# Kernel optimization log

Measured on AMD Instinct MI355X. Metric: run time of the kernel, lower is better.

The kernel has to match this reference:

```python
import jax, jax.numpy as jnp
import numpy as np

B, S, E = 2, 2048, 2048
H, KV, D = 16, 4, 128
G = H // KV
ROPE_THETA = 10000.0


def setup_inputs() -> dict:
    key = jax.random.key(0)
    ks = jax.random.split(key, 8)
    std = 0.02
    return {
        "x": jax.random.normal(ks[0], (B, S, E), jnp.float32),
        "Wq": jax.random.normal(ks[1], (H * D, E), jnp.float32) * std,
        "bq": jax.random.normal(ks[2], (H * D,), jnp.float32) * std,
        "Wk": jax.random.normal(ks[3], (KV * D, E), jnp.float32) * std,
        "bk": jax.random.normal(ks[4], (KV * D,), jnp.float32) * std,
        "Wv": jax.random.normal(ks[5], (KV * D, E), jnp.float32) * std,
        "bv": jax.random.normal(ks[6], (KV * D,), jnp.float32) * std,
        "Wo": jax.random.normal(ks[7], (E, H * D), jnp.float32) * std,
    }


def _rope_cos_sin(seq_len, head_dim):
    inv_freq = 1.0 / (ROPE_THETA ** (jnp.arange(0, head_dim, 2, dtype=jnp.float32) / head_dim))
    pos = jnp.arange(seq_len, dtype=jnp.float32)  # rope scale factor = 1.0
    freqs = pos[:, None] * inv_freq[None, :]        # [S, D/2]
    emb = jnp.concatenate([freqs, freqs], axis=-1)  # [S, D]
    return jnp.cos(emb), jnp.sin(emb)


def _apply_rope(t, cos, sin):
    # t: [..., S, <extra dims>, D]; cos/sin: [S, D] broadcast over extra dims
    half = t.shape[-1] // 2
    extra = t.ndim - 3  # dims between S (axis 1) and D (last)
    c = cos.reshape((1, cos.shape[0]) + (1,) * extra + (cos.shape[1],))
    s = sin.reshape((1, sin.shape[0]) + (1,) * extra + (sin.shape[1],))
    rot = jnp.concatenate([-t[..., half:], t[..., :half]], axis=-1)
    return t * c + rot * s


def reference(x, Wq, bq, Wk, bk, Wv, bv, Wo):
    b, s, e = x.shape
    # QKV projections (biases on q/k/v, none on o)
    q = (jnp.einsum("bse,he->bsh", x, Wq) + bq).reshape(b, s, KV, G, D)
    k = (jnp.einsum("bse,he->bsh", x, Wk) + bk).reshape(b, s, KV, D)
    v = (jnp.einsum("bse,he->bsh", x, Wv) + bv).reshape(b, s, KV, D)

    cos, sin = _rope_cos_sin(s, D)
    q = _apply_rope(q, cos, sin)
    k = _apply_rope(k, cos, sin)

    scale = 1.0 / jnp.sqrt(jnp.float32(D))
    # GQA: q heads grouped per kv head; k/v broadcast over group dim
    scores = jnp.einsum("bskgd,btkd->bkgst", q, k) * scale  # [B,KV,G,S,S]
    causal = jnp.tril(jnp.ones((s, s), dtype=bool))
    scores = jnp.where(causal, scores, jnp.float32(-1e9))
    attn = jax.nn.softmax(scores, axis=-1)
    out = jnp.einsum("bkgst,btkd->bskgd", attn, v).reshape(b, s, H * D)
    return jnp.einsum("bsh,eh->bse", out, Wo)
```

## Files before the change

### kernel.cpp

```cpp
#include <hip/hip_runtime.h>
#include <hip/hip_bf16.h>
#include <math.h>

#define BB 2
#define SS 2048
#define EE 2048
#define HH 16
#define KVH 4
#define DD 128
#define QTILES 32

typedef short short8 __attribute__((ext_vector_type(8)));
typedef float f32x4 __attribute__((ext_vector_type(4)));

__device__ __forceinline__ unsigned int f2bf1(float x) {
    union { float f; unsigned int u; } v; v.f = x;
    return (v.u + 0x7FFFu + ((v.u >> 16) & 1u)) >> 16;
}
__device__ __forceinline__ unsigned int packbf(float a, float b) {
    return f2bf1(a) | (f2bf1(b) << 16);
}
__device__ __forceinline__ void gl_lds16(const void* g, void* l) {
    __builtin_amdgcn_global_load_lds(
        (const __attribute__((address_space(1))) unsigned int*)g,
        (__attribute__((address_space(3))) unsigned int*)l,
        16, 0, 0);
}

__global__ __launch_bounds__(256) void cvt_all_kernel(
    const float* __restrict__ x,  const float* __restrict__ Wq,
    const float* __restrict__ Wk, const float* __restrict__ Wv,
    const float* __restrict__ Wo, const float* __restrict__ bq,
    const float* __restrict__ bk, const float* __restrict__ bv,
    unsigned short* __restrict__ xb, unsigned short* __restrict__ wqkv,
    unsigned short* __restrict__ wob, float* __restrict__ bqkv,
    float* __restrict__ rtab)
{
    long id = (long)blockIdx.x * 256 + threadIdx.x;
    const float* src; unsigned short* dst; long j;
    if (id < 2097152)      { j = id;           src = x;  dst = xb; }
    else if (id < 3145728) { j = id - 2097152; src = Wq; dst = wqkv; }
    else if (id < 3407872) { j = id - 3145728; src = Wk; dst = wqkv + 4194304; }
    else if (id < 3670016) { j = id - 3407872; src = Wv; dst = wqkv + 5242880; }
    else if (id < 4718592) { j = id - 3670016; src = Wo; dst = wob; }
    else if (id < 4719360) {
        long c = (id - 4718592) * 4;
#pragma unroll
        for (int e = 0; e < 4; ++e) {
            long cc = c + e;
            bqkv[cc] = (cc < 2048) ? bq[cc] : (cc < 2560 ? bk[cc - 2048] : bv[cc - 2560]);
        }
        return;
    } else if (id < 4850432) {
        long e = id - 4719360;
        int sg = (int)(e >> 6);
        int dg = (int)(e & 63);
        float inv_freq = expf(-(float)dg * (logf(10000.0f) / 64.0f));
        float fr = (float)sg * inv_freq;
        rtab[e]          = cosf(fr);
        rtab[131072 + e] = sinf(fr);
        return;
    } else return;
    float4 f = ((const float4*)src)[j];
    ((uint2*)dst)[j] = make_uint2(packbf(f.x, f.y), packbf(f.z, f.w));
}

template <bool OUT_BF16>
__global__ __launch_bounds__(256) void gemm_mfma_kernel(
    const unsigned short* __restrict__ A, const unsigned short* __restrict__ W,
    const float* __restrict__ bias, void* __restrict__ Cout,
    int M, int N, int K)
{
    __shared__ unsigned short As[128 * 32];
    __shared__ unsigned short Bs[128 * 32];

    const int tid  = threadIdx.x;
    const int w    = tid >> 6;
    const int lane = tid & 63;
    const int quad = lane >> 4;
    const int l16  = lane & 15;
    const int wr   = w >> 1, wc = w & 1;
    const int m0 = blockIdx.y * 128, n0 = blockIdx.x * 128;

    f32x4 acc[4][4];
#pragma unroll
    for (int i = 0; i < 4; ++i)
#pragma unroll
        for (int j = 0; j < 4; ++j) acc[i][j] = (f32x4){0.f, 0.f, 0.f, 0.f};

    const unsigned short* Ag = A + (size_t)(m0 + w * 32 + (lane >> 2)) * K + (lane & 3) * 8;
    const unsigned short* Wg = W + (size_t)(n0 + w * 32 + (lane >> 2)) * K + (lane & 3) * 8;
    unsigned short* AsB = &As[(w * 32) * 32];
    unsigned short* BsB = &Bs[(w * 32) * 32];

    for (int k0 = 0; k0 < K; k0 += 32) {
        gl_lds16(Ag + k0, AsB);
        gl_lds16(Ag + k0 + (size_t)16 * K, AsB + 16 * 32);
        gl_lds16(Wg + k0, BsB);
        gl_lds16(Wg + k0 + (size_t)16 * K, BsB + 16 * 32);
        __syncthreads();

        short8 a_f[4], b_f[4];
#pragma unroll
        for (int i = 0; i < 4; ++i)
            a_f[i] = *(const short8*)&As[(wr * 64 + i * 16 + l16) * 32 + quad * 8];
#pragma unroll
        for (int j = 0; j < 4; ++j)
            b_f[j] = *(const short8*)&Bs[(wc * 64 + j * 16 + l16) * 32 + quad * 8];
#pragma unroll
        for (int i = 0; i < 4; ++i)
#pragma unroll
            for (int j = 0; j < 4; ++j)
                acc[i][j] = __builtin_amdgcn_mfma_f32_16x16x32_bf16(a_f[i], b_f[j], acc[i][j], 0, 0, 0);
        __syncthreads();
    }

    float bj[4];
#pragma unroll
    for (int j = 0; j < 4; ++j)
        bj[j] = bias ? bias[n0 + wc * 64 + j * 16 + l16] : 0.0f;
#pragma unroll
    for (int i = 0; i < 4; ++i) {
#pragma unroll
        for (int r = 0; r < 4; ++r) {
            size_t row = m0 + wr * 64 + i * 16 + quad * 4 + r;
#pragma unroll
            for (int j = 0; j < 4; ++j) {
                size_t col = n0 + wc * 64 + j * 16 + l16;
                float val = acc[i][j][r] + bj[j];
                if (OUT_BF16)
                    ((unsigned short*)Cout)[row * N + col] = (unsigned short)f2bf1(val);
                else
                    ((float*)Cout)[row * N + col] = val;
            }
        }
    }
}

__global__ __launch_bounds__(256) void rope_kernel(
    unsigned short* __restrict__ qkv,
    const float* __restrict__ ctab, const float* __restrict__ stab)
{
    const int m = blockIdx.x;
    const int s = m & (SS - 1);
    unsigned short* p = qkv + (size_t)m * 3072;
    const float* cr = ctab + s * 64;
    const float* sr = stab + s * 64;
#pragma unroll
    for (int it = 0; it < 5; ++it) {
        int idx = threadIdx.x + it * 256;
        int hh = idx >> 6;
        int d  = idx & 63;
        int cb = (hh < 16) ? hh * 128 : 2048 + (hh - 16) * 128;
        float c  = cr[d];
        float sn = sr[d];
        union { unsigned int u; float f; } x1, x2;
        x1.u = ((unsigned int)p[cb + d]) << 16;
        x2.u = ((unsigned int)p[cb + d + 64]) << 16;
        p[cb + d]      = (unsigned short)f2bf1(x1.f * c - x2.f * sn);
        p[cb + d + 64] = (unsigned short)f2bf1(x2.f * c + x1.f * sn);
    }
}

__global__ __launch_bounds__(256, 2) void attn_mfma_kernel(
    const unsigned short* __restrict__ qkv, unsigned short* __restrict__ o)
{
    __shared__ unsigned int Ks_u[2][64 * 64];
    __shared__ unsigned int Vs_u[2][128 * 32];
    __shared__ unsigned short Ps[4][16 * 64];

    const int tid  = threadIdx.x;
    const int w    = tid >> 6;
    const int lane = tid & 63;
    const int quad = lane >> 4;
    const int l16  = lane & 15;
    const int jpair = blockIdx.x;
    const int h     = blockIdx.y;
    const int b     = blockIdx.z;
    const int kv    = h >> 2;

    const float k2 = 0.12752789744920764f;

    const unsigned short* kbase = qkv + (size_t)b * SS * 3072 + 2048 + kv * 128;
    const unsigned short* vbase = kbase + 512;

    const int kc  = tid & 15;
    const int kp0 = tid >> 4;
    const int vpp = tid >> 3;
    const int vd0 = (tid & 7) * 16;

    for (int pass = 0; pass < 2; ++pass) {
        const int qt = pass ? (QTILES - 1 - jpair) : jpair;
        const int q0 = qt * 64;

        short8 qf[4];
        {
            const unsigned short* qp = qkv + (size_t)(b * SS + q0 + w * 16 + l16) * 3072 + h * 128 + quad * 8;
#pragma unroll
            for (int ks = 0; ks < 4; ++ks)
                qf[ks] = *(const short8*)(qp + ks * 32);
        }

        uint4 kpre[4], vpa[2], vpb[2];
        {
            const unsigned short* kg = kbase + (size_t)kp0 * 3072 + kc * 8;
#pragma unroll
            for (int rr = 0; rr < 4; ++rr)
                kpre[rr] = *(const uint4*)(kg + (size_t)rr * 16 * 3072);
            const unsigned short* vg = vbase + (size_t)(2 * vpp) * 3072 + vd0;
            vpa[0] = *(const uint4*)(vg);
            vpa[1] = *(const uint4*)(vg + 8);
            vpb[0] = *(const uint4*)(vg + 3072);
            vpb[1] = *(const uint4*)(vg + 3072 + 8);
        }

        float m_r[4], l_r[4];
        f32x4 Oacc[8];
#pragma unroll
        for (int r = 0; r < 4; ++r) { m_r[r] = -1e30f; l_r[r] = 0.0f; }
#pragma unroll
        for (int ot = 0; ot < 8; ++ot) Oacc[ot] = (f32x4){0.f, 0.f, 0.f, 0.f};

        for (int t = 0; t <= qt; ++t) {
            const int buf = t & 1;
            unsigned int* Kb = Ks_u[buf];
            unsigned int* Vb = Vs_u[buf];

#pragma unroll
            for (int rr = 0; rr < 4; ++rr) {
                int pos = kp0 + rr * 16;
                int key = (kp0 + rr) & 7;
                *(uint4*)&Kb[pos * 64 + (kc ^ key) * 4] = kpre[rr];
            }
            {
                const unsigned int* pa = (const unsigned int*)vpa;
                const unsigned int* pb = (const unsigned int*)vpb;
#pragma unroll
                for (int j = 0; j < 8; ++j) {
                    unsigned lo = __builtin_amdgcn_perm(pb[j], pa[j], 0x05040100);
                    unsigned hi = __builtin_amdgcn_perm(pb[j], pa[j], 0x07060302);
                    int d0 = vd0 + 2 * j;
                    int g  = d0 >> 4;
                    int k0 = (d0 + g) & 7;
                    int k1 = (d0 + 1 + g) & 7;
                    Vb[d0 * 32 + (((vpp >> 2) ^ k0) & 7) * 4 + (vpp & 3)] = lo;
                    Vb[(d0 + 1) * 32 + (((vpp >> 2) ^ k1) & 7) * 4 + (vpp & 3)] = hi;
                }
            }

            if (t < qt) {
                const unsigned short* kg = kbase + (size_t)((t + 1) * 64 + kp0) * 3072 + kc * 8;
#pragma unroll
                for (int rr = 0; rr < 4; ++rr)
                    kpre[rr] = *(const uint4*)(kg + (size_t)rr * 16 * 3072);
                const unsigned short* vg = vbase + (size_t)((t + 1) * 64 + 2 * vpp) * 3072 + vd0;
                vpa[0] = *(const uint4*)(vg);
                vpa[1] = *(const uint4*)(vg + 8);
                vpb[0] = *(const uint4*)(vg + 3072);
                vpb[1] = *(const uint4*)(vg + 3072 + 8);
            }
            __syncthreads();

            f32x4 S[4];
#pragma unroll
            for (int ct = 0; ct < 4; ++ct) {
                f32x4 s = (f32x4){0.f, 0.f, 0.f, 0.f};
                const int row = ct * 16 + l16;
                const int key = (l16 + ct) & 7;
#pragma unroll
                for (int ks = 0; ks < 4; ++ks) {
                    short8 kf = *(const short8*)&Kb[row * 64 + ((ks * 4 + quad) ^ key) * 4];
                    s = __builtin_amdgcn_mfma_f32_16x16x32_bf16(qf[ks], kf, s, 0, 0, 0);
                }
                S[ct] = s;
            }

            if (t == qt) {
                const int rowloc = w * 16 + quad * 4;
#pragma unroll
                for (int ct = 0; ct < 4; ++ct)
#pragma unroll
                    for (int r = 0; r < 4; ++r)
                        if (ct * 16 + l16 > rowloc + r) S[ct][r] = -1e30f;
            }

#pragma unroll
            for (int r = 0; r < 4; ++r) {
                float c0 = fmaxf(fmaxf(S[0][r], S[1][r]), fmaxf(S[2][r], S[3][r]));
                c0 = fmaxf(c0, __shfl_xor(c0, 1));
                c0 = fmaxf(c0, __shfl_xor(c0, 2));
                c0 = fmaxf(c0, __shfl_xor(c0, 4));
                c0 = fmaxf(c0, __shfl_xor(c0, 8));
                float mnew = fmaxf(m_r[r], c0);
                float alpha = exp2f((m_r[r] - mnew) * k2);
                m_r[r] = mnew;
                float mh = mnew * k2;
                float rs = 0.0f;
                const int prow = quad * 4 + r;
                const int pkey = (prow >> 2) ^ ((prow & 3) << 1);
#pragma unroll
                for (int ct = 0; ct < 4; ++ct) {
                    float p = exp2f(S[ct][r] * k2 - mh);
                    rs += p;
                    int chunk = ct * 2 + (l16 >> 3);
                    union { float f; unsigned u; } pu; pu.f = p;
                    Ps[w][prow * 64 + (chunk ^ pkey) * 8 + (l16 & 7)] =
                        (unsigned short)((pu.u + 0x8000u) >> 16);
                }
                rs += __shfl_xor(rs, 1);
                rs += __shfl_xor(rs, 2);
                rs += __shfl_xor(rs, 4);
                rs += __shfl_xor(rs, 8);
                l_r[r] = l_r[r] * alpha + rs;
#pragma unroll
                for (int ot = 0; ot < 8; ++ot) Oacc[ot][r] *= alpha;
            }

            {
                const int pkeyr = (l16 >> 2) ^ ((l16 & 3) << 1);
                short8 pf0 = *(const short8*)&Ps[w][l16 * 64 + (quad ^ pkeyr) * 8];
                short8 pf1 = *(const short8*)&Ps[w][l16 * 64 + ((4 + quad) ^ pkeyr) * 8];
#pragma unroll
                for (int ot = 0; ot < 8; ++ot) {
                    const int d = ot * 16 + l16;
                    const int vkey = (l16 + ot) & 7;
                    short8 v0 = *(const short8*)&Vb[d * 32 + (quad ^ vkey) * 4];
                    Oacc[ot] = __builtin_amdgcn_mfma_f32_16x16x32_bf16(pf0, v0, Oacc[ot], 0, 0, 0);
                    short8 v1 = *(const short8*)&Vb[d * 32 + ((4 + quad) ^ vkey) * 4];
                    Oacc[ot] = __builtin_amdgcn_mfma_f32_16x16x32_bf16(pf1, v1, Oacc[ot], 0, 0, 0);
                }
            }
        }

        float inv[4];
#pragma unroll
        for (int r = 0; r < 4; ++r) inv[r] = 1.0f / l_r[r];
        const int orow0 = q0 + w * 16 + quad * 4;
        unsigned short* ob = o + (size_t)(b * SS + orow0) * 2048 + h * 128 + l16;
#pragma unroll
        for (int r = 0; r < 4; ++r)
#pragma unroll
            for (int ot = 0; ot < 8; ++ot)
                ob[(size_t)r * 2048 + ot * 16] = (unsigned short)f2bf1(Oacc[ot][r] * inv[r]);

        __syncthreads();
    }
}

extern "C" void kernel_launch(void* const* d_in, const int* in_sizes, int n_in,
                              void* d_out, int out_size, void* d_ws, size_t ws_size,
                              hipStream_t stream)
{
    const float* x  = (const float*)d_in[0];
    const float* Wq = (const float*)d_in[1];
    const float* bq = (const float*)d_in[2];
    const float* Wk = (const float*)d_in[3];
    const float* bk = (const float*)d_in[4];
    const float* Wv = (const float*)d_in[5];
    const float* bv = (const float*)d_in[6];
    const float* Wo = (const float*)d_in[7];
    float* out = (float*)d_out;

    const int M = BB * SS;
    char* wsb = (char*)d_ws;
    unsigned short* xb   = (unsigned short*)wsb;  wsb += (size_t)M * EE * 2;
    unsigned short* wqkv = (unsigned short*)wsb;  wsb += (size_t)3072 * EE * 2;
    unsigned short* wob  = (unsigned short*)wsb;  wsb += (size_t)EE * EE * 2;
    unsigned short* qkvb = (unsigned short*)wsb;  wsb += (size_t)M * 3072 * 2;
    unsigned short* abb  = (unsigned short*)wsb;  wsb += (size_t)M * 2048 * 2;
    float* bqkv = (float*)wsb;                    wsb += 4096 * 4;
    float* rtab = (float*)wsb;

    cvt_all_kernel<<<18947, 256, 0, stream>>>(x, Wq, Wk, Wv, Wo, bq, bk, bv,
                                              xb, wqkv, wob, bqkv, rtab);

    gemm_mfma_kernel<true><<<dim3(3072 / 128, M / 128), 256, 0, stream>>>(
        xb, wqkv, bqkv, qkvb, M, 3072, EE);

    rope_kernel<<<M, 256, 0, stream>>>(qkvb, rtab, rtab + 131072);

    attn_mfma_kernel<<<dim3(16, HH, BB), 256, 0, stream>>>(qkvb, abb);

    gemm_mfma_kernel<false><<<dim3(EE / 128, M / 128), 256, 0, stream>>>(
        abb, wob, nullptr, out, M, EE, 2048);
}
```

Measured before the change: 361.7 us.

## Split long causal query tiles across two blocks and merge partials

The paired-pass attention grid (16 blocks, each doing a short and a long query tile) becomes 48 blocks. The first 16 query tiles are handled whole, and the last 16 are split into two KV-range halves whose unnormalized outputs and max/sum stats are written to fp32 workspace. A new merge kernel combines each pair with log-sum-exp rescaling. The K/V LDS double buffer is also dropped to a single buffer with an extra barrier, which shrinks LDS use. The cost is an extra launch, fp32 partial traffic, and less overlap between loads and compute.

```diff
diff --git a/kernel.cpp b/kernel.cpp
--- a/kernel.cpp
+++ b/kernel.cpp
@@ -163,10 +163,11 @@
 }
 
 __global__ __launch_bounds__(256, 2) void attn_mfma_kernel(
-    const unsigned short* __restrict__ qkv, unsigned short* __restrict__ o)
-{
-    __shared__ unsigned int Ks_u[2][64 * 64];
-    __shared__ unsigned int Vs_u[2][128 * 32];
+    const unsigned short* __restrict__ qkv, unsigned short* __restrict__ o,
+    float* __restrict__ Opart, float* __restrict__ mlpart)
+{
+    __shared__ unsigned int Ks_u[64 * 64];
+    __shared__ unsigned int Vs_u[128 * 32];
     __shared__ unsigned short Ps[4][16 * 64];
 
     const int tid  = threadIdx.x;
@@ -174,10 +175,25 @@
     const int lane = tid & 63;
     const int quad = lane >> 4;
     const int l16  = lane & 15;
-    const int jpair = blockIdx.x;
     const int h     = blockIdx.y;
     const int b     = blockIdx.z;
     const int kv    = h >> 2;
+
+    const int x = blockIdx.x;
+    int qt, tbeg, tend, nc, ch;
+    if (x < 16) {
+        qt = x; tbeg = 0; tend = qt + 1; nc = 1; ch = 0;
+    } else {
+        int i = x - 16;
+        qt = 16 + (i >> 1);
+        ch = i & 1;
+        int len = qt + 1;
+        int half = (len + 1) >> 1;
+        tbeg = ch ? half : 0;
+        tend = ch ? len : half;
+        nc = 2;
+    }
+    const int q0 = qt * 64;
 
     const float k2 = 0.12752789744920764f;
 
@@ -189,149 +205,147 @@
     const int vpp = tid >> 3;
     const int vd0 = (tid & 7) * 16;
 
-    for (int pass = 0; pass < 2; ++pass) {
-        const int qt = pass ? (QTILES - 1 - jpair) : jpair;
-        const int q0 = qt * 64;
-
-        short8 qf[4];
+    unsigned int* Kb = Ks_u;
+    unsigned int* Vb = Vs_u;
+
+    short8 qf[4];
+    {
+        const unsigned short* qp = qkv + (size_t)(b * SS + q0 + w * 16 + l16) * 3072 + h * 128 + quad * 8;
+#pragma unroll
+        for (int ks = 0; ks < 4; ++ks)
+            qf[ks] = *(const short8*)(qp + ks * 32);
+    }
+
+    uint4 kpre[4], vpa[2], vpb[2];
+    {
+        const unsigned short* kg = kbase + (size_t)(tbeg * 64 + kp0) * 3072 + kc * 8;
+#pragma unroll
+        for (int rr = 0; rr < 4; ++rr)
+            kpre[rr] = *(const uint4*)(kg + (size_t)rr * 16 * 3072);
+        const unsigned short* vg = vbase + (size_t)(tbeg * 64 + 2 * vpp) * 3072 + vd0;
+        vpa[0] = *(const uint4*)(vg);
+        vpa[1] = *(const uint4*)(vg + 8);
+        vpb[0] = *(const uint4*)(vg + 3072);
+        vpb[1] = *(const uint4*)(vg + 3072 + 8);
+    }
+
+    float m_r[4], l_r[4];
+    f32x4 Oacc[8];
+#pragma unroll
+    for (int r = 0; r < 4; ++r) { m_r[r] = -1e30f; l_r[r] = 0.0f; }
+#pragma unroll
+    for (int ot = 0; ot < 8; ++ot) Oacc[ot] = (f32x4){0.f, 0.f, 0.f, 0.f};
+
+    for (int t = tbeg; t < tend; ++t) {
+        __syncthreads();
+
+#pragma unroll
+        for (int rr = 0; rr < 4; ++rr) {
+            int pos = kp0 + rr * 16;
+            int key = (kp0 + rr) & 7;
+            *(uint4*)&Kb[pos * 64 + (kc ^ key) * 4] = kpre[rr];
+        }
         {
-            const unsigned short* qp = qkv + (size_t)(b * SS + q0 + w * 16 + l16) * 3072 + h * 128 + quad * 8;
-#pragma unroll
-            for (int ks = 0; ks < 4; ++ks)
-                qf[ks] = *(const short8*)(qp + ks * 32);
-        }
-
-        uint4 kpre[4], vpa[2], vpb[2];
-        {
-            const unsigned short* kg = kbase + (size_t)kp0 * 3072 + kc * 8;
+            const unsigned int* pa = (const unsigned int*)vpa;
+            const unsigned int* pb = (const unsigned int*)vpb;
+#pragma unroll
+            for (int j = 0; j < 8; ++j) {
+                unsigned lo = __builtin_amdgcn_perm(pb[j], pa[j], 0x05040100);
+                unsigned hi = __builtin_amdgcn_perm(pb[j], pa[j], 0x07060302);
+                int d0 = vd0 + 2 * j;
+                int g  = d0 >> 4;
+                int k0 = (d0 + g) & 7;
+                int k1 = (d0 + 1 + g) & 7;
+                Vb[d0 * 32 + (((vpp >> 2) ^ k0) & 7) * 4 + (vpp & 3)] = lo;
+                Vb[(d0 + 1) * 32 + (((vpp >> 2) ^ k1) & 7) * 4 + (vpp & 3)] = hi;
+            }
+        }
+
+        if (t + 1 < tend) {
+            const unsigned short* kg = kbase + (size_t)((t + 1) * 64 + kp0) * 3072 + kc * 8;
 #pragma unroll
             for (int rr = 0; rr < 4; ++rr)
                 kpre[rr] = *(const uint4*)(kg + (size_t)rr * 16 * 3072);
-            const unsigned short* vg = vbase + (size_t)(2 * vpp) * 3072 + vd0;
+            const unsigned short* vg = vbase + (size_t)((t + 1) * 64 + 2 * vpp) * 3072 + vd0;
             vpa[0] = *(const uint4*)(vg);
             vpa[1] = *(const uint4*)(vg + 8);
             vpb[0] = *(const uint4*)(vg + 3072);
             vpb[1] = *(const uint4*)(vg + 3072 + 8);
         }
-
-        float m_r[4], l_r[4];
-        f32x4 Oacc[8];
-#pragma unroll
-        for (int r = 0; r < 4; ++r) { m_r[r] = -1e30f; l_r[r] = 0.0f; }
-#pragma unroll
-        for (int ot = 0; ot < 8; ++ot) Oacc[ot] = (f32x4){0.f, 0.f, 0.f, 0.f};
-
-        for (int t = 0; t <= qt; ++t) {
-            const int buf = t & 1;
-            unsigned int* Kb = Ks_u[buf];
-            unsigned int* Vb = Vs_u[buf];
-
-#pragma unroll
-            for (int rr = 0; rr < 4; ++rr) {
-                int pos = kp0 + rr * 16;
-                int key = (kp0 + rr) & 7;
-                *(uint4*)&Kb[pos * 64 + (kc ^ key) * 4] = kpre[rr];
-            }
-            {
-                const unsigned int* pa = (const unsigned int*)vpa;
-                const unsigned int* pb = (const unsigned int*)vpb;
-#pragma unroll
-                for (int j = 0; j < 8; ++j) {
-                    unsigned lo = __builtin_amdgcn_perm(pb[j], pa[j], 0x05040100);
-                    unsigned hi = __builtin_amdgcn_perm(pb[j], pa[j], 0x07060302);
-                    int d0 = vd0 + 2 * j;
-                    int g  = d0 >> 4;
-                    int k0 = (d0 + g) & 7;
-                    int k1 = (d0 + 1 + g) & 7;
-                    Vb[d0 * 32 + (((vpp >> 2) ^ k0) & 7) * 4 + (vpp & 3)] = lo;
-                    Vb[(d0 + 1) * 32 + (((vpp >> 2) ^ k1) & 7) * 4 + (vpp & 3)] = hi;
-                }
-            }
-
-            if (t < qt) {
-                const unsigned short* kg = kbase + (size_t)((t + 1) * 64 + kp0) * 3072 + kc * 8;
-#pragma unroll
-                for (int rr = 0; rr < 4; ++rr)
-                    kpre[rr] = *(const uint4*)(kg + (size_t)rr * 16 * 3072);
-                const unsigned short* vg = vbase + (size_t)((t + 1) * 64 + 2 * vpp) * 3072 + vd0;
-                vpa[0] = *(const uint4*)(vg);
-                vpa[1] = *(const uint4*)(vg + 8);
-                vpb[0] = *(const uint4*)(vg + 3072);
-                vpb[1] = *(const uint4*)(vg + 3072 + 8);
-            }
-            __syncthreads();
-
-            f32x4 S[4];
+        __syncthreads();
+
+        f32x4 S[4];
+#pragma unroll
+        for (int ct = 0; ct < 4; ++ct) {
+            f32x4 s = (f32x4){0.f, 0.f, 0.f, 0.f};
+            const int row = ct * 16 + l16;
+            const int key = (l16 + ct) & 7;
+#pragma unroll
+            for (int ks = 0; ks < 4; ++ks) {
+                short8 kf = *(const short8*)&Kb[row * 64 + ((ks * 4 + quad) ^ key) * 4];
+                s = __builtin_amdgcn_mfma_f32_16x16x32_bf16(qf[ks], kf, s, 0, 0, 0);
+            }
+            S[ct] = s;
+        }
+
+        if (t == qt) {
+            const int rowloc = w * 16 + quad * 4;
+#pragma unroll
+            for (int ct = 0; ct < 4; ++ct)
+#pragma unroll
+                for (int r = 0; r < 4; ++r)
+                    if (ct * 16 + l16 > rowloc + r) S[ct][r] = -1e30f;
+        }
+
+#pragma unroll
+        for (int r = 0; r < 4; ++r) {
+            float c0 = fmaxf(fmaxf(S[0][r], S[1][r]), fmaxf(S[2][r], S[3][r]));
+            c0 = fmaxf(c0, __shfl_xor(c0, 1));
+            c0 = fmaxf(c0, __shfl_xor(c0, 2));
+            c0 = fmaxf(c0, __shfl_xor(c0, 4));
+            c0 = fmaxf(c0, __shfl_xor(c0, 8));
+            float mnew = fmaxf(m_r[r], c0);
+            float alpha = exp2f((m_r[r] - mnew) * k2);
+            m_r[r] = mnew;
+            float mh = mnew * k2;
+            float rs = 0.0f;
+            const int prow = quad * 4 + r;
+            const int pkey = (prow >> 2) ^ ((prow & 3) << 1);
 #pragma unroll
             for (int ct = 0; ct < 4; ++ct) {
-                f32x4 s = (f32x4){0.f, 0.f, 0.f, 0.f};
-                const int row = ct * 16 + l16;
-                const int key = (l16 + ct) & 7;
-#pragma unroll
-                for (int ks = 0; ks < 4; ++ks) {
-                    short8 kf = *(const short8*)&Kb[row * 64 + ((ks * 4 + quad) ^ key) * 4];
-                    s = __builtin_amdgcn_mfma_f32_16x16x32_bf16(qf[ks], kf, s, 0, 0, 0);
-                }
-                S[ct] = s;
-            }
-
-            if (t == qt) {
-                const int rowloc = w * 16 + quad * 4;
-#pragma unroll
-                for (int ct = 0; ct < 4; ++ct)
-#pragma unroll
-                    for (int r = 0; r < 4; ++r)
-                        if (ct * 16 + l16 > rowloc + r) S[ct][r] = -1e30f;
-            }
-
-#pragma unroll
-            for (int r = 0; r < 4; ++r) {
-                float c0 = fmaxf(fmaxf(S[0][r], S[1][r]), fmaxf(S[2][r], S[3][r]));
-                c0 = fmaxf(c0, __shfl_xor(c0, 1));
-                c0 = fmaxf(c0, __shfl_xor(c0, 2));
-                c0 = fmaxf(c0, __shfl_xor(c0, 4));
-                c0 = fmaxf(c0, __shfl_xor(c0, 8));
-                float mnew = fmaxf(m_r[r], c0);
-                float alpha = exp2f((m_r[r] - mnew) * k2);
-                m_r[r] = mnew;
-                float mh = mnew * k2;
-                float rs = 0.0f;
-                const int prow = quad * 4 + r;
-                const int pkey = (prow >> 2) ^ ((prow & 3) << 1);
-#pragma unroll
-                for (int ct = 0; ct < 4; ++ct) {
-                    float p = exp2f(S[ct][r] * k2 - mh);
-                    rs += p;
-                    int chunk = ct * 2 + (l16 >> 3);
-                    union { float f; unsigned u; } pu; pu.f = p;
-                    Ps[w][prow * 64 + (chunk ^ pkey) * 8 + (l16 & 7)] =
-                        (unsigned short)((pu.u + 0x8000u) >> 16);
-                }
-                rs += __shfl_xor(rs, 1);
-                rs += __shfl_xor(rs, 2);
-                rs += __shfl_xor(rs, 4);
-                rs += __shfl_xor(rs, 8);
-                l_r[r] = l_r[r] * alpha + rs;
-#pragma unroll
-                for (int ot = 0; ot < 8; ++ot) Oacc[ot][r] *= alpha;
-            }
-
-            {
-                const int pkeyr = (l16 >> 2) ^ ((l16 & 3) << 1);
-                short8 pf0 = *(const short8*)&Ps[w][l16 * 64 + (quad ^ pkeyr) * 8];
-                short8 pf1 = *(const short8*)&Ps[w][l16 * 64 + ((4 + quad) ^ pkeyr) * 8];
-#pragma unroll
-                for (int ot = 0; ot < 8; ++ot) {
-                    const int d = ot * 16 + l16;
-                    const int vkey = (l16 + ot) & 7;
-                    short8 v0 = *(const short8*)&Vb[d * 32 + (quad ^ vkey) * 4];
-                    Oacc[ot] = __builtin_amdgcn_mfma_f32_16x16x32_bf16(pf0, v0, Oacc[ot], 0, 0, 0);
-                    short8 v1 = *(const short8*)&Vb[d * 32 + ((4 + quad) ^ vkey) * 4];
-                    Oacc[ot] = __builtin_amdgcn_mfma_f32_16x16x32_bf16(pf1, v1, Oacc[ot], 0, 0, 0);
-                }
-            }
-        }
-
+                float p = exp2f(S[ct][r] * k2 - mh);
+                rs += p;
+                int chunk = ct * 2 + (l16 >> 3);
+                union { float f; unsigned u; } pu; pu.f = p;
+                Ps[w][prow * 64 + (chunk ^ pkey) * 8 + (l16 & 7)] =
+                    (unsigned short)((pu.u + 0x8000u) >> 16);
+            }
+            rs += __shfl_xor(rs, 1);
+            rs += __shfl_xor(rs, 2);
+            rs += __shfl_xor(rs, 4);
+            rs += __shfl_xor(rs, 8);
+            l_r[r] = l_r[r] * alpha + rs;
+#pragma unroll
+            for (int ot = 0; ot < 8; ++ot) Oacc[ot][r] *= alpha;
+        }
+
+        {
+            const int pkeyr = (l16 >> 2) ^ ((l16 & 3) << 1);
+            short8 pf0 = *(const short8*)&Ps[w][l16 * 64 + (quad ^ pkeyr) * 8];
+            short8 pf1 = *(const short8*)&Ps[w][l16 * 64 + ((4 + quad) ^ pkeyr) * 8];
+#pragma unroll
+            for (int ot = 0; ot < 8; ++ot) {
+                const int d = ot * 16 + l16;
+                const int vkey = (l16 + ot) & 7;
+                short8 v0 = *(const short8*)&Vb[d * 32 + (quad ^ vkey) * 4];
+                Oacc[ot] = __builtin_amdgcn_mfma_f32_16x16x32_bf16(pf0, v0, Oacc[ot], 0, 0, 0);
+                short8 v1 = *(const short8*)&Vb[d * 32 + ((4 + quad) ^ vkey) * 4];
+                Oacc[ot] = __builtin_amdgcn_mfma_f32_16x16x32_bf16(pf1, v1, Oacc[ot], 0, 0, 0);
+            }
+        }
+    }
+
+    if (nc == 1) {
         float inv[4];
 #pragma unroll
         for (int r = 0; r < 4; ++r) inv[r] = 1.0f / l_r[r];
@@ -342,8 +356,58 @@
 #pragma unroll
             for (int ot = 0; ot < 8; ++ot)
                 ob[(size_t)r * 2048 + ot * 16] = (unsigned short)f2bf1(Oacc[ot][r] * inv[r]);
-
-        __syncthreads();
+    } else {
+        const int pidx = (((b * HH + h) * 16) + (qt - 16)) * 2 + ch;
+        float* Op = Opart + (size_t)pidx * (64 * 128);
+        const int rowloc0 = w * 16 + quad * 4;
+#pragma unroll
+        for (int r = 0; r < 4; ++r)
+#pragma unroll
+            for (int ot = 0; ot < 8; ++ot)
+                Op[(size_t)(rowloc0 + r) * 128 + ot * 16 + l16] = Oacc[ot][r];
+        if (l16 == 0) {
+            float* mlp = mlpart + (size_t)pidx * 128;
+#pragma unroll
+            for (int r = 0; r < 4; ++r) {
+                mlp[rowloc0 + r]      = m_r[r];
+                mlp[64 + rowloc0 + r] = l_r[r];
+            }
+        }
+    }
+}
+
+__global__ __launch_bounds__(256) void attn_merge_kernel(
+    const float* __restrict__ Opart, const float* __restrict__ mlpart,
+    unsigned short* __restrict__ o)
+{
+    const float k2 = 0.12752789744920764f;
+    const int qt = 16 + blockIdx.x;
+    const int h  = blockIdx.y;
+    const int b  = blockIdx.z;
+    const int pbase = (((b * HH + h) * 16) + (qt - 16)) * 2;
+    const float* O0  = Opart + (size_t)pbase * (64 * 128);
+    const float* O1  = O0 + 64 * 128;
+    const float* ml0 = mlpart + (size_t)pbase * 128;
+    const float* ml1 = ml0 + 128;
+
+    const int g = threadIdx.x >> 6;
+    const int c = threadIdx.x & 63;
+
+#pragma unroll
+    for (int it = 0; it < 16; ++it) {
+        int row = g + it * 4;
+        float m0 = ml0[row], m1 = ml1[row];
+        float l0 = ml0[64 + row], l1 = ml1[64 + row];
+        float M  = fmaxf(m0, m1);
+        float w0 = exp2f((m0 - M) * k2);
+        float w1 = exp2f((m1 - M) * k2);
+        float inv = 1.0f / (w0 * l0 + w1 * l1);
+        const float* p0 = O0 + row * 128 + c * 2;
+        const float* p1 = O1 + row * 128 + c * 2;
+        float a = (w0 * p0[0] + w1 * p1[0]) * inv;
+        float bv2 = (w0 * p0[1] + w1 * p1[1]) * inv;
+        unsigned int* ob = (unsigned int*)(o + (size_t)(b * SS + qt * 64 + row) * 2048 + h * 128) + c;
+        *ob = packbf(a, bv2);
     }
 }
 
@@ -369,7 +433,9 @@
     unsigned short* qkvb = (unsigned short*)wsb;  wsb += (size_t)M * 3072 * 2;
     unsigned short* abb  = (unsigned short*)wsb;  wsb += (size_t)M * 2048 * 2;
     float* bqkv = (float*)wsb;                    wsb += 4096 * 4;
-    float* rtab = (float*)wsb;
+    float* rtab = (float*)wsb;                    wsb += (size_t)2 * 131072 * 4;
+    float* Opart = (float*)wsb;                   wsb += (size_t)1024 * 64 * 128 * 4;
+    float* mlpart = (float*)wsb;
 
     cvt_all_kernel<<<18947, 256, 0, stream>>>(x, Wq, Wk, Wv, Wo, bq, bk, bv,
                                               xb, wqkv, wob, bqkv, rtab);
@@ -379,7 +445,9 @@
 
     rope_kernel<<<M, 256, 0, stream>>>(qkvb, rtab, rtab + 131072);
 
-    attn_mfma_kernel<<<dim3(16, HH, BB), 256, 0, stream>>>(qkvb, abb);
+    attn_mfma_kernel<<<dim3(48, HH, BB), 256, 0, stream>>>(qkvb, abb, Opart, mlpart);
+
+    attn_merge_kernel<<<dim3(16, HH, BB), 256, 0, stream>>>(Opart, mlpart, abb);
 
     gemm_mfma_kernel<false><<<dim3(EE / 128, M / 128), 256, 0, stream>>>(
         abb, wob, nullptr, out, M, EE, 2048);
```

After: 429.0 us. 1.19x slower.
